# Kernel optimization log

Hardware: AMD Instinct MI355X
Metric: run time of the kernel (lower is better)

Reference implementation:

```python
import jax, jax.numpy as jnp
import numpy as np

N = 100000      # nodes
E = 640000      # edges
VOCAB = 100     # Embedding(num_embeddings=100)
EMB = 10        # embed_dim
H = 128         # GCN hidden width


def gcn_conv(x, W, b, src, dst, n):
    """PyG GCNConv: linear (no bias) -> add self loops -> sym-normalized scatter-add -> +bias."""
    x = x @ W                                  # [n, out]
    loop = jnp.arange(n, dtype=src.dtype)
    src2 = jnp.concatenate([src, loop])        # [E+n]
    dst2 = jnp.concatenate([dst, loop])
    deg = jax.ops.segment_sum(jnp.ones_like(dst2, dtype=x.dtype), dst2, num_segments=n)
    dinv = jnp.where(deg > 0, jax.lax.rsqrt(deg), 0.0)
    norm = dinv[src2] * dinv[dst2]             # [E+n]
    out = jax.ops.segment_sum(x[src2] * norm[:, None], dst2, num_segments=n)
    return out + b


def setup_inputs() -> dict:
    key = jax.random.key(0)
    ks = jax.random.split(key, 9)
    x = jax.random.randint(ks[0], (N, 1), 0, VOCAB, dtype=jnp.int32)
    edge_index = jax.random.randint(ks[1], (2, E), 0, N, dtype=jnp.int32)
    batch = jnp.zeros((N,), dtype=jnp.int32)
    emb = jax.random.normal(ks[2], (VOCAB, EMB), dtype=jnp.float32)
    W1 = jax.random.normal(ks[3], (EMB, H), dtype=jnp.float32) * 0.1
    b1 = jnp.zeros((H,), dtype=jnp.float32)
    W2 = jax.random.normal(ks[4], (H, H), dtype=jnp.float32) * 0.1
    b2 = jnp.zeros((H,), dtype=jnp.float32)
    W3 = jax.random.normal(ks[5], (H, 1), dtype=jnp.float32) * 0.1
    b3 = jnp.zeros((1,), dtype=jnp.float32)
    return {"x": x, "edge_index": edge_index, "batch": batch,
            "emb": emb, "W1": W1, "b1": b1, "W2": W2, "b2": b2, "W3": W3, "b3": b3}


def reference(x, edge_index, batch, emb, W1, b1, W2, b2, W3, b3):
    # eval mode: dropout(p=0.5) is identity
    h = emb[x[:, 0]]                           # [N, EMB] embedding lookup + squeeze
    src, dst = edge_index[0], edge_index[1]
    n = h.shape[0]
    h = jax.nn.relu(gcn_conv(h, W1, b1, src, dst, n))   # [N, 128]
    h = jax.nn.relu(gcn_conv(h, W2, b2, src, dst, n))   # [N, 128]
    out = jax.nn.sigmoid((h @ W3 + b3).reshape(-1))      # [N]
    return out
```

## Files before the change

### kernel.cpp

```cpp
#include <hip/hip_runtime.h>
#include <math.h>

#define HDIM 128
#define EMBD 10
#define CAP  64
#define ZSTRIDE 136

typedef __attribute__((ext_vector_type(8))) short short8;
typedef __attribute__((ext_vector_type(8))) unsigned short ushort8;
typedef __attribute__((ext_vector_type(4))) float float4a;

__device__ inline ushort bf16_rne(float f) {
    unsigned u = __float_as_uint(f);
    unsigned r = (u + 0x7fffu + ((u >> 16) & 1u)) >> 16;
    return (ushort)r;
}
__device__ inline float bf16_to_f(ushort u) {
    return __uint_as_float(((unsigned)u) << 16);
}

__global__ void k_prep(const float* __restrict__ emb, const float* __restrict__ W1,
                       const float* __restrict__ W2, ushort* __restrict__ Tb,
                       ushort* __restrict__ W2t, int* __restrict__ cnt,
                       int N, int vocab) {
    int t = blockIdx.x * 256 + threadIdx.x;
    if (t < N) cnt[t] = 0;
    if (t < vocab * HDIM) {
        int c = t >> 7, f = t & 127;
        float s = 0.f;
#pragma unroll
        for (int k = 0; k < EMBD; ++k) s += emb[c * EMBD + k] * W1[k * HDIM + f];
        Tb[t] = bf16_rne(s);
    }
    if (t < HDIM * HDIM) {
        int n = t >> 7, k = t & 127;
        W2t[t] = bf16_rne(W2[k * HDIM + n]);
    }
}

__global__ void k_fill(const int* __restrict__ src, const int* __restrict__ dst,
                       int* __restrict__ cnt, int* __restrict__ slot, int E) {
    int e = blockIdx.x * blockDim.x + threadIdx.x;
    if (e >= E) return;
    int d = dst[e];
    int p = atomicAdd(&cnt[d], 1);
    if (p < CAP) slot[(size_t)d * CAP + p] = src[e];
}

__global__ void k_meta(const int* __restrict__ x, const int* __restrict__ cnt,
                       unsigned* __restrict__ meta, int N) {
    int v = blockIdx.x * 256 + threadIdx.x;
    if (v >= N) return;
    meta[v] = ((unsigned)x[v] << 16) | (unsigned)bf16_rne(rsqrtf((float)cnt[v] + 1.0f));
}

__global__ __launch_bounds__(512) void k_gather1(const int* __restrict__ slot,
                                                 const int* __restrict__ cnt,
                                                 const unsigned* __restrict__ meta,
                                                 const ushort* __restrict__ Tb,
                                                 const float* __restrict__ b1,
                                                 ushort* __restrict__ Ap,
                                                 int N, int vocab) {
    __shared__ ushort TbL[100 * HDIM];
    int n8 = (vocab * HDIM) >> 3;
    for (int i = threadIdx.x; i < n8; i += 512)
        ((ushort8*)TbL)[i] = ((const ushort8*)Tb)[i];
    __syncthreads();

    int tid = blockIdx.x * 512 + threadIdx.x;
    int v = tid >> 4, q = tid & 15;
    if (v >= N) return;
    int deg = cnt[v];
    int m = min(deg, CAP);
    float dv = rsqrtf((float)deg + 1.0f);

    unsigned mv = meta[(q < m) ? slot[(size_t)v * CAP + q] : v];
    int cq = mv >> 16;
    float wq = (q < m) ? bf16_to_f((ushort)(mv & 0xffffu))
                       : ((q == m) ? dv : 0.f);

    float acc[8] = {0.f, 0.f, 0.f, 0.f, 0.f, 0.f, 0.f, 0.f};
#pragma unroll
    for (int t = 0; t < 16; ++t) {
        int c = __shfl(cq, t, 16);
        float ww = __shfl(wq, t, 16);
        ushort8 y = *(const ushort8*)&TbL[c * HDIM + q * 8];
#pragma unroll
        for (int k = 0; k < 8; ++k) acc[k] += ww * bf16_to_f(y[k]);
    }
    for (int base = 16; base < m; base += 16) {
        int j = base + q;
        unsigned mj = meta[(j < m) ? slot[(size_t)v * CAP + j] : v];
        int cj = mj >> 16;
        float wj = (j < m) ? bf16_to_f((ushort)(mj & 0xffffu)) : 0.f;
#pragma unroll
        for (int t = 0; t < 16; ++t) {
            int c = __shfl(cj, t, 16);
            float ww = __shfl(wj, t, 16);
            ushort8 y = *(const ushort8*)&TbL[c * HDIM + q * 8];
#pragma unroll
            for (int k = 0; k < 8; ++k) acc[k] += ww * bf16_to_f(y[k]);
        }
    }
    if (m >= 16) {
        int c = meta[v] >> 16;
        ushort8 y = *(const ushort8*)&TbL[c * HDIM + q * 8];
#pragma unroll
        for (int k = 0; k < 8; ++k) acc[k] += dv * bf16_to_f(y[k]);
    }
    float4 bb0 = *(const float4*)(b1 + q * 8);
    float4 bb1 = *(const float4*)(b1 + q * 8 + 4);
    float bb[8] = {bb0.x, bb0.y, bb0.z, bb0.w, bb1.x, bb1.y, bb1.z, bb1.w};
    ushort8 o;
#pragma unroll
    for (int k = 0; k < 8; ++k)
        o[k] = bf16_rne(dv * fmaxf(dv * acc[k] + bb[k], 0.f));
    *(ushort8*)(Ap + (size_t)v * HDIM + q * 8) = o;
}

__global__ __launch_bounds__(256, 4) void k_conv2(const int* __restrict__ slot,
                                                  const int* __restrict__ cnt,
                                                  const ushort* __restrict__ Ap,
                                                  const ushort* __restrict__ W2t,
                                                  const float* __restrict__ b2,
                                                  const float* __restrict__ W3,
                                                  const float* __restrict__ b3,
                                                  float* __restrict__ out, int N) {
    __shared__ ushort Z[16 * ZSTRIDE];
    __shared__ float pbuf[4][16];
    int tid = threadIdx.x;
    int g = tid >> 4, q = tid & 15;
    int v0 = blockIdx.x * 16;
    int v = min(v0 + g, N - 1);

    int deg = cnt[v];
    int m = min(deg, CAP);
    float dv = rsqrtf((float)deg + 1.0f);

    int sq = (q < m) ? slot[(size_t)v * CAP + q] : v;

    ushort8 rows[16];
#pragma unroll
    for (int t = 0; t < 16; ++t) {
        int s = __shfl(sq, t, 16);
        rows[t] = *(const ushort8*)(Ap + (size_t)s * HDIM + q * 8);
    }
    float acc[8] = {0.f, 0.f, 0.f, 0.f, 0.f, 0.f, 0.f, 0.f};
#pragma unroll
    for (int t = 0; t < 16; ++t) {
        float wt = (t <= m) ? 1.f : 0.f;
#pragma unroll
        for (int k = 0; k < 8; ++k) acc[k] += wt * bf16_to_f(rows[t][k]);
    }
    for (int base = 16; base < m; base += 16) {
        int j = base + q;
        int sj = (j < m) ? slot[(size_t)v * CAP + j] : v;
#pragma unroll
        for (int t = 0; t < 16; ++t) {
            int s = __shfl(sj, t, 16);
            float wt = (base + t < m) ? 1.f : 0.f;
            ushort8 y = *(const ushort8*)(Ap + (size_t)s * HDIM + q * 8);
#pragma unroll
            for (int k = 0; k < 8; ++k) acc[k] += wt * bf16_to_f(y[k]);
        }
    }
    if (m >= 16) {
        ushort8 y = *(const ushort8*)(Ap + (size_t)v * HDIM + q * 8);
#pragma unroll
        for (int k = 0; k < 8; ++k) acc[k] += bf16_to_f(y[k]);
    }
    ushort8 z;
#pragma unroll
    for (int k = 0; k < 8; ++k) z[k] = bf16_rne(dv * acc[k]);
    *(ushort8*)&Z[g * ZSTRIDE + q * 8] = z;
    __syncthreads();

    int lane = tid & 63, w = tid >> 6;
    int l15 = lane & 15, g4 = lane >> 4;
    short8 af[4];
#pragma unroll
    for (int kt = 0; kt < 4; ++kt)
        af[kt] = *(const short8*)&Z[l15 * ZSTRIDE + kt * 32 + g4 * 8];

    float pr[4] = {0.f, 0.f, 0.f, 0.f};
#pragma unroll
    for (int i = 0; i < 2; ++i) {
        int nt = w * 2 + i;
        int col = nt * 16 + l15;
        const ushort* bp = W2t + (size_t)col * HDIM + g4 * 8;
        float4a accD = {0.f, 0.f, 0.f, 0.f};
#pragma unroll
        for (int kt = 0; kt < 4; ++kt) {
            short8 bf = *(const short8*)(bp + kt * 32);
            accD = __builtin_amdgcn_mfma_f32_16x16x32_bf16(af[kt], bf, accD, 0, 0, 0);
        }
        float bc = b2[col], wc = W3[col];
#pragma unroll
        for (int r = 0; r < 4; ++r)
            pr[r] += fmaxf(accD[r] + bc, 0.f) * wc;
    }
#pragma unroll
    for (int off = 1; off < 16; off <<= 1) {
#pragma unroll
        for (int r = 0; r < 4; ++r) pr[r] += __shfl_xor(pr[r], off, 16);
    }
    if (l15 == 0) {
#pragma unroll
        for (int r = 0; r < 4; ++r) pbuf[w][g4 * 4 + r] = pr[r];
    }
    __syncthreads();
    if (tid < 16) {
        int row = tid;
        float s = pbuf[0][row] + pbuf[1][row] + pbuf[2][row] + pbuf[3][row];
        int vr = v0 + row;
        if (vr < N) out[vr] = 1.f / (1.f + expf(-(s + b3[0])));
    }
}

extern "C" void kernel_launch(void* const* d_in, const int* in_sizes, int n_in,
                              void* d_out, int out_size, void* d_ws, size_t ws_size,
                              hipStream_t stream) {
    const int*   x    = (const int*)d_in[0];
    const int*   ei   = (const int*)d_in[1];
    const float* emb  = (const float*)d_in[3];
    const float* W1   = (const float*)d_in[4];
    const float* b1   = (const float*)d_in[5];
    const float* W2   = (const float*)d_in[6];
    const float* b2   = (const float*)d_in[7];
    const float* W3   = (const float*)d_in[8];
    const float* b3   = (const float*)d_in[9];
    float*       out  = (float*)d_out;

    int N = in_sizes[0];
    int E = in_sizes[1] / 2;
    int vocab = in_sizes[3] / EMBD;
    const int* src = ei;
    const int* dst = ei + E;

    char* w = (char*)d_ws;
    ushort*   Tb   = (ushort*)w;    w += (size_t)vocab * HDIM * 2;
    ushort*   Ap   = (ushort*)w;    w += (size_t)N * HDIM * 2;
    ushort*   W2t  = (ushort*)w;    w += (size_t)HDIM * HDIM * 2;
    int*      cnt  = (int*)w;       w += (size_t)N * 4;
    unsigned* meta = (unsigned*)w;  w += (size_t)N * 4;
    int*      slot = (int*)w;       w += (size_t)N * CAP * 4;

    int prep_elems = N;
    if (vocab * HDIM > prep_elems) prep_elems = vocab * HDIM;
    if (HDIM * HDIM > prep_elems) prep_elems = HDIM * HDIM;
    k_prep<<<(prep_elems + 255) / 256, 256, 0, stream>>>(emb, W1, W2, Tb, W2t, cnt, N, vocab);
    k_fill<<<(E + 255) / 256, 256, 0, stream>>>(src, dst, cnt, slot, E);
    k_meta<<<(N + 255) / 256, 256, 0, stream>>>(x, cnt, meta, N);

    int g1blocks = (int)(((long long)N * 16 + 511) / 512);
    k_gather1<<<g1blocks, 512, 0, stream>>>(slot, cnt, meta, Tb, b1, Ap, N, vocab);

    int cblocks = (N + 15) / 16;
    k_conv2<<<cblocks, 256, 0, stream>>>(slot, cnt, Ap, W2t, b2, W3, b3, out, N);
}
```

Measured before the change: 179.9 us.

## Assign one wavefront per node in both gather kernels with 4-way edge splitting

Both aggregation kernels now map a full 64-lane wavefront to each node instead of a 16-lane group. The four 16-lane sub-groups each take every fourth neighbour and are then combined with cross-lane xor shuffles. Layer one also drops its shared-memory copy of the embedding table and reads the table directly from global memory through cache. Layer two processes 8 nodes per 512-thread block, zero-pads the unused half of the MFMA input tile, and gives each wave one 16-column output tile. The goal is less per-thread serial work on high-degree nodes and fewer wasted lanes, at the cost of more blocks, more shuffles and half-empty MFMA tiles.

```diff
diff --git a/kernel.cpp b/kernel.cpp
--- a/kernel.cpp
+++ b/kernel.cpp
@@ -54,165 +54,128 @@
     meta[v] = ((unsigned)x[v] << 16) | (unsigned)bf16_rne(rsqrtf((float)cnt[v] + 1.0f));
 }
 
-__global__ __launch_bounds__(512) void k_gather1(const int* __restrict__ slot,
+__global__ __launch_bounds__(256) void k_gather1(const int* __restrict__ slot,
                                                  const int* __restrict__ cnt,
                                                  const unsigned* __restrict__ meta,
                                                  const ushort* __restrict__ Tb,
                                                  const float* __restrict__ b1,
-                                                 ushort* __restrict__ Ap,
-                                                 int N, int vocab) {
-    __shared__ ushort TbL[100 * HDIM];
-    int n8 = (vocab * HDIM) >> 3;
-    for (int i = threadIdx.x; i < n8; i += 512)
-        ((ushort8*)TbL)[i] = ((const ushort8*)Tb)[i];
-    __syncthreads();
-
-    int tid = blockIdx.x * 512 + threadIdx.x;
-    int v = tid >> 4, q = tid & 15;
-    if (v >= N) return;
+                                                 ushort* __restrict__ Ap, int N) {
+    int tid = threadIdx.x;
+    int wv = tid >> 6, lane = tid & 63;
+    int q = lane & 15, j = lane >> 4;
+    int v = blockIdx.x * 4 + wv;
+    if (v >= N) v = N - 1;
     int deg = cnt[v];
     int m = min(deg, CAP);
     float dv = rsqrtf((float)deg + 1.0f);
 
-    unsigned mv = meta[(q < m) ? slot[(size_t)v * CAP + q] : v];
-    int cq = mv >> 16;
-    float wq = (q < m) ? bf16_to_f((ushort)(mv & 0xffffu))
-                       : ((q == m) ? dv : 0.f);
-
     float acc[8] = {0.f, 0.f, 0.f, 0.f, 0.f, 0.f, 0.f, 0.f};
-#pragma unroll
-    for (int t = 0; t < 16; ++t) {
-        int c = __shfl(cq, t, 16);
-        float ww = __shfl(wq, t, 16);
-        ushort8 y = *(const ushort8*)&TbL[c * HDIM + q * 8];
-#pragma unroll
-        for (int k = 0; k < 8; ++k) acc[k] += ww * bf16_to_f(y[k]);
-    }
-    for (int base = 16; base < m; base += 16) {
-        int j = base + q;
-        unsigned mj = meta[(j < m) ? slot[(size_t)v * CAP + j] : v];
-        int cj = mj >> 16;
-        float wj = (j < m) ? bf16_to_f((ushort)(mj & 0xffffu)) : 0.f;
-#pragma unroll
-        for (int t = 0; t < 16; ++t) {
-            int c = __shfl(cj, t, 16);
-            float ww = __shfl(wj, t, 16);
-            ushort8 y = *(const ushort8*)&TbL[c * HDIM + q * 8];
-#pragma unroll
-            for (int k = 0; k < 8; ++k) acc[k] += ww * bf16_to_f(y[k]);
-        }
-    }
-    if (m >= 16) {
-        int c = meta[v] >> 16;
-        ushort8 y = *(const ushort8*)&TbL[c * HDIM + q * 8];
-#pragma unroll
-        for (int k = 0; k < 8; ++k) acc[k] += dv * bf16_to_f(y[k]);
-    }
-    float4 bb0 = *(const float4*)(b1 + q * 8);
-    float4 bb1 = *(const float4*)(b1 + q * 8 + 4);
-    float bb[8] = {bb0.x, bb0.y, bb0.z, bb0.w, bb1.x, bb1.y, bb1.z, bb1.w};
-    ushort8 o;
-#pragma unroll
-    for (int k = 0; k < 8; ++k)
-        o[k] = bf16_rne(dv * fmaxf(dv * acc[k] + bb[k], 0.f));
-    *(ushort8*)(Ap + (size_t)v * HDIM + q * 8) = o;
-}
-
-__global__ __launch_bounds__(256, 4) void k_conv2(const int* __restrict__ slot,
-                                                  const int* __restrict__ cnt,
-                                                  const ushort* __restrict__ Ap,
-                                                  const ushort* __restrict__ W2t,
-                                                  const float* __restrict__ b2,
-                                                  const float* __restrict__ W3,
-                                                  const float* __restrict__ b3,
-                                                  float* __restrict__ out, int N) {
+    int total = m + 1;
+    for (int base = 0; base < total; base += 4) {
+        int idx = base + j;
+        int s = (idx < m) ? slot[(size_t)v * CAP + idx] : v;
+        unsigned mv = meta[s];
+        float wt = (idx <= m) ? bf16_to_f((ushort)(mv & 0xffffu)) : 0.f;
+        ushort8 y = *(const ushort8*)(Tb + (size_t)(mv >> 16) * HDIM + q * 8);
+#pragma unroll
+        for (int k = 0; k < 8; ++k) acc[k] += wt * bf16_to_f(y[k]);
+    }
+#pragma unroll
+    for (int k = 0; k < 8; ++k) {
+        acc[k] += __shfl_xor(acc[k], 16, 64);
+        acc[k] += __shfl_xor(acc[k], 32, 64);
+    }
+    if (j == 0) {
+        float4 bb0 = *(const float4*)(b1 + q * 8);
+        float4 bb1 = *(const float4*)(b1 + q * 8 + 4);
+        float bb[8] = {bb0.x, bb0.y, bb0.z, bb0.w, bb1.x, bb1.y, bb1.z, bb1.w};
+        ushort8 o;
+#pragma unroll
+        for (int k = 0; k < 8; ++k)
+            o[k] = bf16_rne(dv * fmaxf(dv * acc[k] + bb[k], 0.f));
+        *(ushort8*)(Ap + (size_t)v * HDIM + q * 8) = o;
+    }
+}
+
+__global__ __launch_bounds__(512) void k_conv2(const int* __restrict__ slot,
+                                               const int* __restrict__ cnt,
+                                               const ushort* __restrict__ Ap,
+                                               const ushort* __restrict__ W2t,
+                                               const float* __restrict__ b2,
+                                               const float* __restrict__ W3,
+                                               const float* __restrict__ b3,
+                                               float* __restrict__ out, int N) {
     __shared__ ushort Z[16 * ZSTRIDE];
-    __shared__ float pbuf[4][16];
+    __shared__ float pbuf[8][8];
     int tid = threadIdx.x;
-    int g = tid >> 4, q = tid & 15;
-    int v0 = blockIdx.x * 16;
-    int v = min(v0 + g, N - 1);
+    int wv = tid >> 6, lane = tid & 63;
+    int q = lane & 15, j = lane >> 4;
+    int v0 = blockIdx.x * 8;
+    int v = min(v0 + wv, N - 1);
+
+    for (int i = tid; i < (8 * ZSTRIDE) / 8; i += 512)
+        ((ushort8*)&Z[8 * ZSTRIDE])[i] = (ushort8)0;
 
     int deg = cnt[v];
     int m = min(deg, CAP);
     float dv = rsqrtf((float)deg + 1.0f);
 
-    int sq = (q < m) ? slot[(size_t)v * CAP + q] : v;
-
-    ushort8 rows[16];
-#pragma unroll
-    for (int t = 0; t < 16; ++t) {
-        int s = __shfl(sq, t, 16);
-        rows[t] = *(const ushort8*)(Ap + (size_t)s * HDIM + q * 8);
-    }
     float acc[8] = {0.f, 0.f, 0.f, 0.f, 0.f, 0.f, 0.f, 0.f};
-#pragma unroll
-    for (int t = 0; t < 16; ++t) {
-        float wt = (t <= m) ? 1.f : 0.f;
-#pragma unroll
-        for (int k = 0; k < 8; ++k) acc[k] += wt * bf16_to_f(rows[t][k]);
-    }
-    for (int base = 16; base < m; base += 16) {
-        int j = base + q;
-        int sj = (j < m) ? slot[(size_t)v * CAP + j] : v;
-#pragma unroll
-        for (int t = 0; t < 16; ++t) {
-            int s = __shfl(sj, t, 16);
-            float wt = (base + t < m) ? 1.f : 0.f;
-            ushort8 y = *(const ushort8*)(Ap + (size_t)s * HDIM + q * 8);
-#pragma unroll
-            for (int k = 0; k < 8; ++k) acc[k] += wt * bf16_to_f(y[k]);
-        }
-    }
-    if (m >= 16) {
-        ushort8 y = *(const ushort8*)(Ap + (size_t)v * HDIM + q * 8);
-#pragma unroll
-        for (int k = 0; k < 8; ++k) acc[k] += bf16_to_f(y[k]);
-    }
-    ushort8 z;
-#pragma unroll
-    for (int k = 0; k < 8; ++k) z[k] = bf16_rne(dv * acc[k]);
-    *(ushort8*)&Z[g * ZSTRIDE + q * 8] = z;
+    int total = m + 1;
+    for (int base = 0; base < total; base += 4) {
+        int idx = base + j;
+        int s = (idx < m) ? slot[(size_t)v * CAP + idx] : v;
+        float wt = (idx <= m) ? 1.f : 0.f;
+        ushort8 y = *(const ushort8*)(Ap + (size_t)s * HDIM + q * 8);
+#pragma unroll
+        for (int k = 0; k < 8; ++k) acc[k] += wt * bf16_to_f(y[k]);
+    }
+#pragma unroll
+    for (int k = 0; k < 8; ++k) {
+        acc[k] += __shfl_xor(acc[k], 16, 64);
+        acc[k] += __shfl_xor(acc[k], 32, 64);
+    }
+    if (j == 0) {
+        ushort8 z;
+#pragma unroll
+        for (int k = 0; k < 8; ++k) z[k] = bf16_rne(dv * acc[k]);
+        *(ushort8*)&Z[wv * ZSTRIDE + q * 8] = z;
+    }
     __syncthreads();
 
-    int lane = tid & 63, w = tid >> 6;
     int l15 = lane & 15, g4 = lane >> 4;
     short8 af[4];
 #pragma unroll
     for (int kt = 0; kt < 4; ++kt)
         af[kt] = *(const short8*)&Z[l15 * ZSTRIDE + kt * 32 + g4 * 8];
 
-    float pr[4] = {0.f, 0.f, 0.f, 0.f};
-#pragma unroll
-    for (int i = 0; i < 2; ++i) {
-        int nt = w * 2 + i;
-        int col = nt * 16 + l15;
-        const ushort* bp = W2t + (size_t)col * HDIM + g4 * 8;
-        float4a accD = {0.f, 0.f, 0.f, 0.f};
-#pragma unroll
-        for (int kt = 0; kt < 4; ++kt) {
-            short8 bf = *(const short8*)(bp + kt * 32);
-            accD = __builtin_amdgcn_mfma_f32_16x16x32_bf16(af[kt], bf, accD, 0, 0, 0);
-        }
-        float bc = b2[col], wc = W3[col];
-#pragma unroll
-        for (int r = 0; r < 4; ++r)
-            pr[r] += fmaxf(accD[r] + bc, 0.f) * wc;
-    }
+    int col = wv * 16 + l15;
+    const ushort* bp = W2t + (size_t)col * HDIM + g4 * 8;
+    float4a accD = {0.f, 0.f, 0.f, 0.f};
+#pragma unroll
+    for (int kt = 0; kt < 4; ++kt) {
+        short8 bf = *(const short8*)(bp + kt * 32);
+        accD = __builtin_amdgcn_mfma_f32_16x16x32_bf16(af[kt], bf, accD, 0, 0, 0);
+    }
+    float bc = b2[col], wc = W3[col];
+    float pr[4];
+#pragma unroll
+    for (int r = 0; r < 4; ++r) pr[r] = fmaxf(accD[r] + bc, 0.f) * wc;
 #pragma unroll
     for (int off = 1; off < 16; off <<= 1) {
 #pragma unroll
         for (int r = 0; r < 4; ++r) pr[r] += __shfl_xor(pr[r], off, 16);
     }
-    if (l15 == 0) {
-#pragma unroll
-        for (int r = 0; r < 4; ++r) pbuf[w][g4 * 4 + r] = pr[r];
+    if (l15 == 0 && g4 < 2) {
+#pragma unroll
+        for (int r = 0; r < 4; ++r) pbuf[wv][g4 * 4 + r] = pr[r];
     }
     __syncthreads();
-    if (tid < 16) {
-        int row = tid;
-        float s = pbuf[0][row] + pbuf[1][row] + pbuf[2][row] + pbuf[3][row];
-        int vr = v0 + row;
+    if (tid < 8) {
+        float s = 0.f;
+#pragma unroll
+        for (int w = 0; w < 8; ++w) s += pbuf[w][tid];
+        int vr = v0 + tid;
         if (vr < N) out[vr] = 1.f / (1.f + expf(-(s + b3[0])));
     }
 }
@@ -252,9 +215,6 @@
     k_fill<<<(E + 255) / 256, 256, 0, stream>>>(src, dst, cnt, slot, E);
     k_meta<<<(N + 255) / 256, 256, 0, stream>>>(x, cnt, meta, N);
 
-    int g1blocks = (int)(((long long)N * 16 + 511) / 512);
-    k_gather1<<<g1blocks, 512, 0, stream>>>(slot, cnt, meta, Tb, b1, Ap, N, vocab);
-
-    int cblocks = (N + 15) / 16;
-    k_conv2<<<cblocks, 256, 0, stream>>>(slot, cnt, Ap, W2t, b2, W3, b3, out, N);
-}
+    k_gather1<<<(N + 3) / 4, 256, 0, stream>>>(slot, cnt, meta, Tb, b1, Ap, N);
+    k_conv2<<<(N + 7) / 8, 512, 0, stream>>>(slot, cnt, Ap, W2t, b2, W3, b3, out, N);
+}
```

Result: slower. 236.8 us (+31.6%).
